# Kernel tuning notes

Measured on AMD Instinct MI355X. Metric: run time of the kernel, lower is better.

## Reference

```python
import jax, jax.numpy as jnp
import numpy as np

B, D_IN, D_H = 8192, 512, 1024


def setup_inputs() -> dict:
    key = jax.random.key(0)
    ks = jax.random.split(key, 5)
    # Kaiming-normal-ish init: std = sqrt(2/fan_in)
    Wx = jax.random.normal(ks[0], (D_IN, 4 * D_H), jnp.float32) * np.sqrt(2.0 / D_IN)
    Wh = jax.random.normal(ks[1], (D_H, 4 * D_H), jnp.float32) * np.sqrt(2.0 / D_H)
    b = jnp.zeros((4 * D_H,), jnp.float32)
    x = jax.random.normal(ks[2], (B, D_IN), jnp.float32)
    h = jax.random.normal(ks[3], (B, D_H), jnp.float32)
    c = jax.random.normal(ks[4], (B, D_H), jnp.float32)
    return {"x": x, "h": h, "c": c, "Wx": Wx, "Wh": Wh, "b": b}


def reference(x, h, c, Wx, Wh, b):
    # Fused gate pre-activations: [B, 4H] in gate order (g, i, f, o)
    gates = x @ Wx + h @ Wh + b[None, :]
    g_in, i_in, f_in, o_in = jnp.split(gates, 4, axis=-1)
    g_out = jnp.tanh(g_in)
    i_out = jax.nn.sigmoid(i_in)
    # NOTE: faithful to the original source's bug — f_out and o_out both use i_in.
    f_out = jax.nn.sigmoid(i_in)
    o_out = jax.nn.sigmoid(i_in)
    c_new = g_out * i_out + f_out * c
    h_new = jnp.tanh(c_new) * o_out
    return h_new, c_new
```

## Files before the change

### kernel.cpp

```cpp
#include <hip/hip_runtime.h>
#include <hip/hip_bf16.h>
#include <cstdint>

#define BROWS 8192
#define DIN   512
#define DH    1024
#define KTOT  1536

typedef __bf16 bf16x8 __attribute__((ext_vector_type(8)));
typedef __bf16 bf16x4 __attribute__((ext_vector_type(4)));
typedef float  f32x4  __attribute__((ext_vector_type(4)));

__device__ __forceinline__ void load16_to_lds(const void* gptr, void* lptr) {
    __builtin_amdgcn_global_load_lds(
        (const __attribute__((address_space(1))) uint32_t*)gptr,
        (__attribute__((address_space(3))) uint32_t*)lptr,
        16, 0, 0);
}

__global__ __launch_bounds__(256) void cvtA_kernel(
    const float* __restrict__ x, const float* __restrict__ h,
    __bf16* __restrict__ A) {
    int t = blockIdx.x * 256 + threadIdx.x;
    int row = t / 384;
    int kg  = (t - row * 384) * 4;
    const float* src = (kg < DIN) ? (x + (size_t)row * DIN + kg)
                                  : (h + (size_t)row * DH + (kg - DIN));
    float4 v = *(const float4*)src;
    bf16x4 o = { (__bf16)v.x, (__bf16)v.y, (__bf16)v.z, (__bf16)v.w };
    *(bf16x4*)(A + (size_t)row * KTOT + kg) = o;
}

__global__ __launch_bounds__(256) void cvtB_kernel(
    const float* __restrict__ Wx, const float* __restrict__ Wh,
    __bf16* __restrict__ Bt) {
    __shared__ float tile[32][33];
    int k0 = blockIdx.x * 32;
    int n0 = blockIdx.y * 32;
    int tx = threadIdx.x;
    int ty = threadIdx.y;
#pragma unroll
    for (int i = 0; i < 4; ++i) {
        int k = k0 + ty + 8 * i;
        float v = (k < DIN) ? Wx[(size_t)k * 4096 + n0 + tx]
                            : Wh[(size_t)(k - DIN) * 4096 + n0 + tx];
        tile[ty + 8 * i][tx] = v;
    }
    __syncthreads();
#pragma unroll
    for (int i = 0; i < 4; ++i) {
        int np = ty + 8 * i;
        Bt[(size_t)(n0 + np) * KTOT + k0 + tx] = (__bf16)tile[tx][np];
    }
}

__global__ __launch_bounds__(256, 2) void lstm_gemm_kernel(
    const __bf16* __restrict__ A,
    const __bf16* __restrict__ Bt,
    const float* __restrict__ bias,
    const float* __restrict__ c_in,
    float* __restrict__ out_h,
    float* __restrict__ out_c) {
    __shared__ __bf16 sA [128][64];
    __shared__ __bf16 sBg[128][64];
    __shared__ __bf16 sBi[128][64];

    const int tid  = threadIdx.x;
    const int lane = tid & 63;
    const int wid  = tid >> 6;
    const int wr   = wid >> 1;
    const int wc   = wid & 1;
    const int brow = blockIdx.x * 128;
    const int bn   = blockIdx.y * 128;

    const int l15 = lane & 15;
    const int l4  = lane >> 4;

    f32x4 accg[4][4], acci[4][4];
#pragma unroll
    for (int mi = 0; mi < 4; ++mi)
#pragma unroll
        for (int ni = 0; ni < 4; ++ni) {
            accg[mi][ni] = (f32x4){0.f, 0.f, 0.f, 0.f};
            acci[mi][ni] = (f32x4){0.f, 0.f, 0.f, 0.f};
        }

    const int sr = tid >> 3;
    const int sc = (tid & 7) * 8;

    for (int kt = 0; kt < KTOT / 64; ++kt) {
        const int kb0 = kt * 64 + sc;
#pragma unroll
        for (int it = 0; it < 4; ++it) {
            int r = it * 32 + sr;
            load16_to_lds(A  + (size_t)(brow + r) * KTOT + kb0, &sA[r][sc]);
            load16_to_lds(Bt + (size_t)(bn + r) * KTOT + kb0, &sBg[r][sc]);
            load16_to_lds(Bt + (size_t)(1024 + bn + r) * KTOT + kb0, &sBi[r][sc]);
        }
        __syncthreads();
#pragma unroll
        for (int kh = 0; kh < 2; ++kh) {
            const int kb = kh * 32 + l4 * 8;
            bf16x8 af[4], bgf[4], bif[4];
#pragma unroll
            for (int mi = 0; mi < 4; ++mi)
                af[mi] = *(const bf16x8*)&sA[wr * 64 + mi * 16 + l15][kb];
#pragma unroll
            for (int ni = 0; ni < 4; ++ni) {
                bgf[ni] = *(const bf16x8*)&sBg[wc * 64 + ni * 16 + l15][kb];
                bif[ni] = *(const bf16x8*)&sBi[wc * 64 + ni * 16 + l15][kb];
            }
#pragma unroll
            for (int mi = 0; mi < 4; ++mi)
#pragma unroll
                for (int ni = 0; ni < 4; ++ni) {
                    accg[mi][ni] = __builtin_amdgcn_mfma_f32_16x16x32_bf16(
                        af[mi], bgf[ni], accg[mi][ni], 0, 0, 0);
                    acci[mi][ni] = __builtin_amdgcn_mfma_f32_16x16x32_bf16(
                        af[mi], bif[ni], acci[mi][ni], 0, 0, 0);
                }
        }
        __syncthreads();
    }

    const int colbase = bn + wc * 64;
    const int rowbase = brow + wr * 64;
#pragma unroll
    for (int mi = 0; mi < 4; ++mi) {
#pragma unroll
        for (int ni = 0; ni < 4; ++ni) {
            const int col = colbase + ni * 16 + l15;
            const float bg = bias[col];
            const float bi = bias[1024 + col];
#pragma unroll
            for (int r = 0; r < 4; ++r) {
                const int row = rowbase + mi * 16 + l4 * 4 + r;
                const float g_in = accg[mi][ni][r] + bg;
                const float i_in = acci[mi][ni][r] + bi;
                const float s  = 1.0f / (1.0f + __expf(-i_in));
                const float t  = tanhf(g_in);
                const float cv = c_in[(size_t)row * DH + col];
                const float cn = s * (t + cv);
                const float hn = tanhf(cn) * s;
                out_h[(size_t)row * DH + col] = hn;
                out_c[(size_t)row * DH + col] = cn;
            }
        }
    }
}

extern "C" void kernel_launch(void* const* d_in, const int* in_sizes, int n_in,
                              void* d_out, int out_size, void* d_ws, size_t ws_size,
                              hipStream_t stream) {
    const float* x  = (const float*)d_in[0];
    const float* h  = (const float*)d_in[1];
    const float* c  = (const float*)d_in[2];
    const float* Wx = (const float*)d_in[3];
    const float* Wh = (const float*)d_in[4];
    const float* b  = (const float*)d_in[5];

    __bf16* A  = (__bf16*)d_ws;
    __bf16* Bt = (__bf16*)((char*)d_ws + (size_t)BROWS * KTOT * 2);

    float* out_h = (float*)d_out;
    float* out_c = out_h + (size_t)BROWS * DH;

    cvtA_kernel<<<(BROWS * KTOT / 4) / 256, 256, 0, stream>>>(x, h, A);
    cvtB_kernel<<<dim3(KTOT / 32, 2048 / 32), dim3(32, 8), 0, stream>>>(Wx, Wh, Bt);
    lstm_gemm_kernel<<<dim3(BROWS / 128, 1024 / 128), 256, 0, stream>>>(
        A, Bt, b, c, out_h, out_c);
}
```

Measured before the change: 101.2 us.

## Rewrite LSTM GEMM with double-buffered swizzled LDS, 256x128 tiles, 8 waves

The GEMM kernel now uses 512-thread blocks with 256-row tiles and double-buffered LDS. Global-to-LDS loads for the next K step are interleaved with the MFMA phases using explicit waitcnt, barriers and setprio. The conversion kernels write A and Bt in an XOR-swizzled layout so LDS fragment reads avoid bank conflicts, and cvtA is widened to 8 elements per thread. The epilogue replaces tanhf with an exp-based formula. The gain is expected from better load/compute overlap and fewer bank conflicts, at the cost of much more complex synchronisation and a small accuracy change in tanh.

```diff
diff --git a/kernel.cpp b/kernel.cpp
--- a/kernel.cpp
+++ b/kernel.cpp
@@ -6,6 +6,7 @@
 #define DIN   512
 #define DH    1024
 #define KTOT  1536
+#define NT    (KTOT / 64)
 
 typedef __bf16 bf16x8 __attribute__((ext_vector_type(8)));
 typedef __bf16 bf16x4 __attribute__((ext_vector_type(4)));
@@ -22,13 +23,17 @@
     const float* __restrict__ x, const float* __restrict__ h,
     __bf16* __restrict__ A) {
     int t = blockIdx.x * 256 + threadIdx.x;
-    int row = t / 384;
-    int kg  = (t - row * 384) * 4;
+    int row = t / 192;
+    int j = t - row * 192;
+    int kg = j * 8;
     const float* src = (kg < DIN) ? (x + (size_t)row * DIN + kg)
                                   : (h + (size_t)row * DH + (kg - DIN));
-    float4 v = *(const float4*)src;
-    bf16x4 o = { (__bf16)v.x, (__bf16)v.y, (__bf16)v.z, (__bf16)v.w };
-    *(bf16x4*)(A + (size_t)row * KTOT + kg) = o;
+    float4 u = *(const float4*)src;
+    float4 v = *(const float4*)(src + 4);
+    bf16x8 o = { (__bf16)u.x, (__bf16)u.y, (__bf16)u.z, (__bf16)u.w,
+                 (__bf16)v.x, (__bf16)v.y, (__bf16)v.z, (__bf16)v.w };
+    int swz = (j * 16) ^ ((row & 7) << 4);
+    *(bf16x8*)((char*)A + (size_t)row * 3072 + swz) = o;
 }
 
 __global__ __launch_bounds__(256) void cvtB_kernel(
@@ -47,34 +52,110 @@
         tile[ty + 8 * i][tx] = v;
     }
     __syncthreads();
-#pragma unroll
-    for (int i = 0; i < 4; ++i) {
-        int np = ty + 8 * i;
-        Bt[(size_t)(n0 + np) * KTOT + k0 + tx] = (__bf16)tile[tx][np];
-    }
-}
-
-__global__ __launch_bounds__(256, 2) void lstm_gemm_kernel(
+    int n = n0 + tx;
+    int kk = ty * 4;
+    bf16x4 o = { (__bf16)tile[kk][tx], (__bf16)tile[kk + 1][tx],
+                 (__bf16)tile[kk + 2][tx], (__bf16)tile[kk + 3][tx] };
+    int swz = ((k0 + kk) * 2) ^ ((n & 7) << 4);
+    *(bf16x4*)((char*)Bt + (size_t)n * 3072 + swz) = o;
+}
+
+
+#define BARRIER  do { __builtin_amdgcn_sched_barrier(0); __builtin_amdgcn_s_barrier(); __builtin_amdgcn_sched_barrier(0); } while (0)
+#define VMW(n)   do { asm volatile("s_waitcnt vmcnt(" #n ")" ::: "memory"); __builtin_amdgcn_sched_barrier(0); } while (0)
+#define LGKM0    do { asm volatile("s_waitcnt lgkmcnt(0)" ::: "memory"); __builtin_amdgcn_sched_barrier(0); } while (0)
+
+#define STAGE_A(buf, mh, kt) do {                                              \
+    const char* g0_ = Ab + (size_t)(brow + (mh) * 128 + r0) * 3072             \
+                         + (size_t)(kt) * 128 + cb;                            \
+    char* l0_ = sAb + (buf) * 32768 + ((mh) * 128 + r0) * 128 + cb;            \
+    load16_to_lds(g0_, l0_);                                                   \
+    load16_to_lds(g0_ + 64 * 3072, l0_ + 64 * 128);                            \
+} while (0)
+
+#define STAGE_B(buf, half, kt) do {                                            \
+    const char* g0_ = Bb + (size_t)((half) * 1024 + bnp + r0) * 3072           \
+                         + (size_t)(kt) * 128 + cb;                            \
+    char* l0_ = sBb + (buf) * 32768 + ((half) * 128 + r0) * 128 + cb;          \
+    load16_to_lds(g0_, l0_);                                                   \
+    load16_to_lds(g0_ + 64 * 3072, l0_ + 64 * 128);                            \
+} while (0)
+
+#define READ_A(dst, c, mh)                                                     \
+    _Pragma("unroll")                                                          \
+    for (int m2_ = 0; m2_ < 2; ++m2_) {                                        \
+        _Pragma("unroll")                                                      \
+        for (int ks_ = 0; ks_ < 2; ++ks_) {                                    \
+            int row_ = wrow + (mh) * 32 + m2_ * 16 + l15;                      \
+            int kb_ = ks_ * 64 + l4x16;                                        \
+            dst[m2_][ks_] = *(const bf16x8*)(sAb + (c) * 32768 + row_ * 128    \
+                                             + (kb_ ^ swzkey));                \
+        }                                                                      \
+    }
+
+#define READ_B(dst, c, half)                                                   \
+    _Pragma("unroll")                                                          \
+    for (int ni_ = 0; ni_ < 4; ++ni_) {                                        \
+        _Pragma("unroll")                                                      \
+        for (int ks_ = 0; ks_ < 2; ++ks_) {                                    \
+            int row_ = (half) * 128 + wcol + ni_ * 16 + l15;                   \
+            int kb_ = ks_ * 64 + l4x16;                                        \
+            dst[ni_][ks_] = *(const bf16x8*)(sBb + (c) * 32768 + row_ * 128    \
+                                             + (kb_ ^ swzkey));                \
+        }                                                                      \
+    }
+
+#define MMA(ACC, MH, AF, BF) do {                                              \
+    __builtin_amdgcn_s_setprio(1);                                             \
+    _Pragma("unroll")                                                          \
+    for (int ks_ = 0; ks_ < 2; ++ks_) {                                        \
+        _Pragma("unroll")                                                      \
+        for (int m2_ = 0; m2_ < 2; ++m2_) {                                    \
+            _Pragma("unroll")                                                  \
+            for (int ni_ = 0; ni_ < 4; ++ni_) {                                \
+                ACC[(MH) * 2 + m2_][ni_] =                                     \
+                    __builtin_amdgcn_mfma_f32_16x16x32_bf16(                   \
+                        AF[m2_][ks_], BF[ni_][ks_], ACC[(MH) * 2 + m2_][ni_],  \
+                        0, 0, 0);                                              \
+            }                                                                  \
+        }                                                                      \
+    }                                                                          \
+    __builtin_amdgcn_s_setprio(0);                                             \
+    __builtin_amdgcn_sched_barrier(0);                                         \
+} while (0)
+
+__global__ __launch_bounds__(512, 2) void lstm_gemm_kernel(
     const __bf16* __restrict__ A,
     const __bf16* __restrict__ Bt,
     const float* __restrict__ bias,
     const float* __restrict__ c_in,
     float* __restrict__ out_h,
     float* __restrict__ out_c) {
-    __shared__ __bf16 sA [128][64];
-    __shared__ __bf16 sBg[128][64];
-    __shared__ __bf16 sBi[128][64];
+    __shared__ __bf16 sA[2][256][64];
+    __shared__ __bf16 sB[2][256][64];
 
     const int tid  = threadIdx.x;
     const int lane = tid & 63;
     const int wid  = tid >> 6;
-    const int wr   = wid >> 1;
-    const int wc   = wid & 1;
-    const int brow = blockIdx.x * 128;
-    const int bn   = blockIdx.y * 128;
-
-    const int l15 = lane & 15;
-    const int l4  = lane >> 4;
+    const int wr   = wid & 3;
+    const int wc   = wid >> 2;
+    const int bid  = blockIdx.x;
+    const int bnp  = (bid & 7) * 128;
+    const int brow = (bid >> 3) * 256;
+
+    const int l15    = lane & 15;
+    const int l4x16  = (lane >> 4) * 16;
+    const int swzkey = (l15 & 7) << 4;
+    const int wrow   = wr * 64;
+    const int wcol   = wc * 64;
+
+    const int r0 = tid >> 3;
+    const int cb = (tid & 7) * 16;
+
+    const char* Ab = (const char*)A;
+    const char* Bb = (const char*)Bt;
+    char* sAb = (char*)&sA[0][0][0];
+    char* sBb = (char*)&sB[0][0][0];
 
     f32x4 accg[4][4], acci[4][4];
 #pragma unroll
@@ -85,63 +166,75 @@
             acci[mi][ni] = (f32x4){0.f, 0.f, 0.f, 0.f};
         }
 
-    const int sr = tid >> 3;
-    const int sc = (tid & 7) * 8;
-
-    for (int kt = 0; kt < KTOT / 64; ++kt) {
-        const int kb0 = kt * 64 + sc;
-#pragma unroll
-        for (int it = 0; it < 4; ++it) {
-            int r = it * 32 + sr;
-            load16_to_lds(A  + (size_t)(brow + r) * KTOT + kb0, &sA[r][sc]);
-            load16_to_lds(Bt + (size_t)(bn + r) * KTOT + kb0, &sBg[r][sc]);
-            load16_to_lds(Bt + (size_t)(1024 + bn + r) * KTOT + kb0, &sBi[r][sc]);
-        }
-        __syncthreads();
-#pragma unroll
-        for (int kh = 0; kh < 2; ++kh) {
-            const int kb = kh * 32 + l4 * 8;
-            bf16x8 af[4], bgf[4], bif[4];
-#pragma unroll
-            for (int mi = 0; mi < 4; ++mi)
-                af[mi] = *(const bf16x8*)&sA[wr * 64 + mi * 16 + l15][kb];
-#pragma unroll
-            for (int ni = 0; ni < 4; ++ni) {
-                bgf[ni] = *(const bf16x8*)&sBg[wc * 64 + ni * 16 + l15][kb];
-                bif[ni] = *(const bf16x8*)&sBi[wc * 64 + ni * 16 + l15][kb];
-            }
-#pragma unroll
-            for (int mi = 0; mi < 4; ++mi)
-#pragma unroll
-                for (int ni = 0; ni < 4; ++ni) {
-                    accg[mi][ni] = __builtin_amdgcn_mfma_f32_16x16x32_bf16(
-                        af[mi], bgf[ni], accg[mi][ni], 0, 0, 0);
-                    acci[mi][ni] = __builtin_amdgcn_mfma_f32_16x16x32_bf16(
-                        af[mi], bif[ni], acci[mi][ni], 0, 0, 0);
-                }
-        }
-        __syncthreads();
-    }
-
-    const int colbase = bn + wc * 64;
-    const int rowbase = brow + wr * 64;
-#pragma unroll
-    for (int mi = 0; mi < 4; ++mi) {
-#pragma unroll
-        for (int ni = 0; ni < 4; ++ni) {
-            const int col = colbase + ni * 16 + l15;
-            const float bg = bias[col];
-            const float bi = bias[1024 + col];
+    bf16x8 aF0[2][2], aF1[2][2], bgF[4][2], biF[4][2];
+
+    STAGE_A(0, 0, 0);
+    STAGE_A(0, 1, 0);
+    STAGE_B(0, 0, 0);
+    STAGE_B(0, 1, 0);
+
+    for (int t = 0; t < NT - 1; ++t) {
+        const int c  = t & 1;
+        const int nb = c ^ 1;
+        VMW(2); BARRIER;
+        READ_A(aF0, c, 0);
+        READ_B(bgF, c, 0);
+        STAGE_A(nb, 0, t + 1);
+        BARRIER; LGKM0;
+        MMA(accg, 0, aF0, bgF);
+        BARRIER;
+        READ_A(aF1, c, 1);
+        STAGE_A(nb, 1, t + 1);
+        BARRIER; LGKM0;
+        MMA(accg, 1, aF1, bgF);
+        VMW(4); BARRIER;
+        READ_B(biF, c, 1);
+        STAGE_B(nb, 0, t + 1);
+        BARRIER; LGKM0;
+        MMA(acci, 0, aF0, biF);
+        BARRIER;
+        STAGE_B(nb, 1, t + 1);
+        BARRIER;
+        MMA(acci, 1, aF1, biF);
+    }
+    {
+        const int c = (NT - 1) & 1;
+        VMW(2); BARRIER;
+        READ_A(aF0, c, 0);
+        READ_B(bgF, c, 0);
+        BARRIER; LGKM0;
+        MMA(accg, 0, aF0, bgF);
+        BARRIER;
+        READ_A(aF1, c, 1);
+        BARRIER; LGKM0;
+        MMA(accg, 1, aF1, bgF);
+        VMW(0); BARRIER;
+        READ_B(biF, c, 1);
+        BARRIER; LGKM0;
+        MMA(acci, 0, aF0, biF);
+        MMA(acci, 1, aF1, biF);
+    }
+
+    const int R0 = brow + wrow;
+    const int C0 = bnp + wcol;
+    const int l4 = lane >> 4;
+#pragma unroll
+    for (int ni = 0; ni < 4; ++ni) {
+        const int col = C0 + ni * 16 + l15;
+        const float bg = bias[col];
+        const float bi = bias[1024 + col];
+#pragma unroll
+        for (int mi = 0; mi < 4; ++mi) {
 #pragma unroll
             for (int r = 0; r < 4; ++r) {
-                const int row = rowbase + mi * 16 + l4 * 4 + r;
+                const int row = R0 + mi * 16 + l4 * 4 + r;
                 const float g_in = accg[mi][ni][r] + bg;
                 const float i_in = acci[mi][ni][r] + bi;
                 const float s  = 1.0f / (1.0f + __expf(-i_in));
-                const float t  = tanhf(g_in);
+                const float tg = 2.0f / (1.0f + __expf(-2.0f * g_in)) - 1.0f;
                 const float cv = c_in[(size_t)row * DH + col];
-                const float cn = s * (t + cv);
-                const float hn = tanhf(cn) * s;
+                const float cn = s * (tg + cv);
+                const float hn = (2.0f / (1.0f + __expf(-2.0f * cn)) - 1.0f) * s;
                 out_h[(size_t)row * DH + col] = hn;
                 out_c[(size_t)row * DH + col] = cn;
             }
@@ -165,8 +258,7 @@
     float* out_h = (float*)d_out;
     float* out_c = out_h + (size_t)BROWS * DH;
 
-    cvtA_kernel<<<(BROWS * KTOT / 4) / 256, 256, 0, stream>>>(x, h, A);
+    cvtA_kernel<<<(BROWS * (KTOT / 8)) / 256, 256, 0, stream>>>(x, h, A);
     cvtB_kernel<<<dim3(KTOT / 32, 2048 / 32), dim3(32, 8), 0, stream>>>(Wx, Wh, Bt);
-    lstm_gemm_kernel<<<dim3(BROWS / 128, 1024 / 128), 256, 0, stream>>>(
-        A, Bt, b, c, out_h, out_c);
-}
+    lstm_gemm_kernel<<<256, 512, 0, stream>>>(A, Bt, b, c, out_h, out_c);
+}
```

After: 82.42 us. 18.5% less time.
